# Kernel optimization log

Measured on AMD Instinct MI355X. Metric: run time of the kernel, lower is better.

## Reference

```python
import jax, jax.numpy as jnp
import numpy as np


def conv1x1(x, w, b):
    # x: (b,c,h,w), w: (o,c), b: (o,)
    return jnp.einsum('oc,bchw->bohw', w, x) + b[None, :, None, None]


def make_grid(b, h, w, outH, outW, scale, offset):
    # Replicates the torch grid construction (align_corners=True style normalization).
    gx = ((jnp.arange(outW, dtype=jnp.float32) + 0.5) / scale - 0.5) * 2.0 / (w - 1) - 1.0
    gy = ((jnp.arange(outH, dtype=jnp.float32) + 0.5) / scale - 0.5) * 2.0 / (h - 1) - 1.0
    ix = jnp.broadcast_to(gx[None, None, :], (b, outH, outW))
    iy = jnp.broadcast_to(gy[None, :, None], (b, outH, outW))
    if offset is not None:
        ix = ix + offset[:, 0] * 2.0 / (w - 1)
        iy = iy + offset[:, 1] * 2.0 / (h - 1)
    return ix, iy


def grid_sample_zeros(img, ix, iy):
    # Bilinear grid_sample, padding_mode='zeros', align_corners=False (torch default).
    b, c, h, w = img.shape
    fx = ((ix + 1.0) * w - 1.0) / 2.0
    fy = ((iy + 1.0) * h - 1.0) / 2.0
    x0 = jnp.floor(fx); y0 = jnp.floor(fy)
    x1 = x0 + 1.0; y1 = y0 + 1.0
    wx1 = fx - x0; wx0 = 1.0 - wx1
    wy1 = fy - y0; wy0 = 1.0 - wy1
    bidx = jnp.arange(b)[:, None, None]

    def gather(xc, yc):
        valid = (xc >= 0) & (xc <= w - 1) & (yc >= 0) & (yc <= h - 1)
        xi = jnp.clip(xc, 0, w - 1).astype(jnp.int32)
        yi = jnp.clip(yc, 0, h - 1).astype(jnp.int32)
        v = img[bidx, :, yi, xi]  # (b,H,W,c)
        return jnp.where(valid[..., None], v, 0.0)

    out = (gather(x0, y0) * (wx0 * wy0)[..., None]
           + gather(x1, y0) * (wx1 * wy0)[..., None]
           + gather(x0, y1) * (wx0 * wy1)[..., None]
           + gather(x1, y1) * (wx1 * wy1)[..., None])
    return jnp.transpose(out, (0, 3, 1, 2))  # (b,c,H,W)


def setup_inputs() -> dict:
    key = jax.random.key(0)
    C, E = 64, 4
    ks = jax.random.split(key, 12)
    s = 0.05
    return {
        'x': jax.random.normal(ks[0], (2, C, 128, 128), dtype=jnp.float32),
        'weight_compress': jax.random.normal(ks[1], (E, C // 8, C), dtype=jnp.float32) * s,
        'weight_expand': jax.random.normal(ks[2], (E, C, C // 8), dtype=jnp.float32) * s,
        'w1': jax.random.normal(ks[3], (C, C + 4), dtype=jnp.float32) * s,
        'b1': jax.random.normal(ks[4], (C,), dtype=jnp.float32) * s,
        'w2': jax.random.normal(ks[5], (C, C), dtype=jnp.float32) * s,
        'b2': jax.random.normal(ks[6], (C,), dtype=jnp.float32) * s,
        'wr': jax.random.normal(ks[7], (E, C), dtype=jnp.float32) * s,
        'br': jax.random.normal(ks[8], (E,), dtype=jnp.float32) * s,
        'wo': jax.random.normal(ks[9], (2, C), dtype=jnp.float32) * s,
        'bo': jax.random.normal(ks[10], (2,), dtype=jnp.float32) * s,
        'scale': 2,
        'outH': 256,
        'outW': 256,
    }


def reference(x, weight_compress, weight_expand, w1, b1, w2, b2, wr, br, wo, bo, scale, outH, outW):
    b, c, h, w = x.shape
    # relative sub-pixel coordinates
    ah = jnp.arange(outH, dtype=jnp.float32)
    aw = jnp.arange(outW, dtype=jnp.float32)
    coor_h = (ah + 0.5) / scale - jnp.floor((ah + 0.5) / scale + 0.001) - 0.5  # (outH,)
    coor_w = (aw + 0.5) / scale - jnp.floor((aw + 0.5) / scale + 0.001) - 0.5  # (outW,)
    ones_hw = jnp.full((outH, outW), 1.0 / scale, dtype=jnp.float32)
    coords = jnp.stack([ones_hw, ones_hw,
                        jnp.broadcast_to(coor_h[:, None], (outH, outW)),
                        jnp.broadcast_to(coor_w[None, :], (outH, outW))], axis=0)  # (4,H,W)
    coords = jnp.broadcast_to(coords[None], (b, 4, outH, outW))

    ix, iy = make_grid(b, h, w, outH, outW, scale, None)
    pre_fea = grid_sample_zeros(x, ix, iy)  # (b,C,H,W)

    inp = jnp.concatenate([coords, pre_fea], axis=1)  # (b,C+4,H,W)
    emb = jax.nn.relu(conv1x1(jax.nn.relu(conv1x1(inp, w1, b1)), w2, b2))

    offset = conv1x1(emb, wo, bo)  # (b,2,H,W)
    ix2, iy2 = make_grid(b, h, w, outH, outW, scale, offset)
    fea0 = grid_sample_zeros(x, ix2, iy2)  # (b,C,H,W)

    r = jax.nn.sigmoid(conv1x1(emb, wr, br))  # (b,E,H,W) routing weights
    # per-pixel expert-blended compress->expand (algebraically identical to
    # materializing per-pixel weight matrices, but as E small GEMM pairs)
    comp = jnp.einsum('behw,edc,bchw->bdhw', r, weight_compress, fea0)  # (b,C/8,H,W)
    out = jnp.einsum('behw,ecd,bdhw->bchw', r, weight_expand, comp)    # (b,C,H,W)
    return out + fea0
```

## Files before the change

### kernel.cpp

```cpp
#include <hip/hip_runtime.h>
#include <math.h>

#define BATCH 2
#define C 64
#define HIN 128
#define WIN 128
#define HW (HIN * WIN)
#define OH 256
#define OW 256

#define BLK 256
#define PIX 64
#define SC 16
#define ASTR 72
#define YSTR 36
#define OSTR 68


typedef __attribute__((ext_vector_type(8))) short bf16x8;
typedef __attribute__((ext_vector_type(4))) float f32x4;

__device__ __forceinline__ unsigned short f2bf(float f) {
    unsigned u = __float_as_uint(f);
    u += 0x7FFFu + ((u >> 16) & 1u);
    return (unsigned short)(u >> 16);
}
__device__ __forceinline__ float bf2f(unsigned short s) {
    return __uint_as_float(((unsigned)s) << 16);
}

__device__ __forceinline__ void bilin_setup(float gx, float gy,
    int& i00, int& i10, int& i01, int& i11,
    float& w00, float& w10, float& w01, float& w11)
{
    const float fx = ((gx + 1.0f) * WIN - 1.0f) * 0.5f;
    const float fy = ((gy + 1.0f) * HIN - 1.0f) * 0.5f;
    const float x0 = floorf(fx), y0 = floorf(fy);
    const float wx1 = fx - x0, wx0 = 1.0f - wx1;
    const float wy1 = fy - y0, wy0 = 1.0f - wy1;
    const float x1 = x0 + 1.0f, y1 = y0 + 1.0f;
    const bool vx0 = (x0 >= 0.0f) && (x0 <= (float)(WIN - 1));
    const bool vx1 = (x1 >= 0.0f) && (x1 <= (float)(WIN - 1));
    const bool vy0 = (y0 >= 0.0f) && (y0 <= (float)(HIN - 1));
    const bool vy1 = (y1 >= 0.0f) && (y1 <= (float)(HIN - 1));
    const int xi0 = (int)fminf(fmaxf(x0, 0.0f), (float)(WIN - 1));
    const int xi1 = (int)fminf(fmaxf(x1, 0.0f), (float)(WIN - 1));
    const int yi0 = (int)fminf(fmaxf(y0, 0.0f), (float)(HIN - 1));
    const int yi1 = (int)fminf(fmaxf(y1, 0.0f), (float)(HIN - 1));
    w00 = wx0 * wy0 * ((vx0 && vy0) ? 1.0f : 0.0f);
    w10 = wx1 * wy0 * ((vx1 && vy0) ? 1.0f : 0.0f);
    w01 = wx0 * wy1 * ((vx0 && vy1) ? 1.0f : 0.0f);
    w11 = wx1 * wy1 * ((vx1 && vy1) ? 1.0f : 0.0f);
    i00 = yi0 * WIN + xi0;  i10 = yi0 * WIN + xi1;
    i01 = yi1 * WIN + xi0;  i11 = yi1 * WIN + xi1;
}

__global__ __launch_bounds__(BLK, 4) void scab_kernel(
    const float* __restrict__ x,
    const float* __restrict__ wcm,
    const float* __restrict__ wex,
    const float* __restrict__ w1,
    const float* __restrict__ b1,
    const float* __restrict__ w2,
    const float* __restrict__ b2,
    const float* __restrict__ wr,
    const float* __restrict__ br,
    const float* __restrict__ wo,
    const float* __restrict__ bo,
    float* __restrict__ out)
{
    __shared__ __align__(16) short act[PIX * ASTR];
    __shared__ __align__(16) float red[PIX * OSTR];

    const int tid  = threadIdx.x;
    const int lane = tid & 63;
    const int s    = __builtin_amdgcn_readfirstlane(tid >> 6);
    const int cb   = s * SC;
    const int l15  = lane & 15;
    const int quad = lane >> 4;
    const int nn   = cb + l15;

    const int gp = blockIdx.x * PIX + lane;
    const int ox = gp & (OW - 1);
    const int oy = (gp >> 8) & (OH - 1);
    const int bb = gp >> 16;

    const float gx = ((ox + 0.5f) * 0.5f - 0.5f) * (2.0f / (WIN - 1)) - 1.0f;
    const float gy = ((oy + 0.5f) * 0.5f - 0.5f) * (2.0f / (HIN - 1)) - 1.0f;

    const float* __restrict__ xb = x + bb * (C * HW);

    bf16x8 bw1[2], bw2[2], bwc[2], bwe;
    {
        const int nt1  = s & 1;
        const int eo_g = nt1 * 16 + l15;
        #pragma unroll
        for (int ks = 0; ks < 2; ++ks) {
            const float* __restrict__ s1p = w1 + nn * (C + 4) + 4 + ks * 32 + quad * 8;
            const float* __restrict__ s2p = w2 + nn * C + ks * 32 + quad * 8;
            const float* __restrict__ scp = wcm + eo_g * C + ks * 32 + quad * 8;
            #pragma unroll
            for (int j = 0; j < 8; ++j) {
                bw1[ks][j] = (short)f2bf(s1p[j]);
                bw2[ks][j] = (short)f2bf(s2p[j]);
                bwc[ks][j] = (short)f2bf(scp[j]);
            }
        }
        const float* __restrict__ sep = wex + (quad * C + nn) * 8;
        #pragma unroll
        for (int j = 0; j < 8; ++j) bwe[j] = (short)f2bf(sep[j]);
    }

    {
        int i00, i10, i01, i11;
        float w00, w10, w01, w11;
        bilin_setup(gx, gy, i00, i10, i01, i11, w00, w10, w01, w11);
        bf16x8 v0, v1;
        #pragma unroll
        for (int kk = 0; kk < SC; kk += 4) {
            float l[16];
            #pragma unroll
            for (int k = 0; k < 4; ++k) {
                const float* __restrict__ xc = xb + (cb + kk + k) * HW;
                l[4*k+0] = xc[i00]; l[4*k+1] = xc[i10];
                l[4*k+2] = xc[i01]; l[4*k+3] = xc[i11];
            }
            #pragma unroll
            for (int k = 0; k < 4; ++k) {
                const float pf = l[4*k]*w00 + l[4*k+1]*w10 + l[4*k+2]*w01 + l[4*k+3]*w11;
                const short b = (short)f2bf(pf);
                if (kk + k < 8) v0[kk + k] = b; else v1[kk + k - 8] = b;
            }
        }
        *(bf16x8*)&act[lane * ASTR + cb]     = v0;
        *(bf16x8*)&act[lane * ASTR + cb + 8] = v1;
    }
    __syncthreads();

    const float coor_h = (oy & 1) ? 0.25f : -0.25f;
    f32x4 acc[4];
    {
        const float4 wh = *(const float4*)(w1 + nn * (C + 4));
        const float qn = b1[nn] + (wh.x + wh.y) * 0.5f + wh.z * coor_h;
        const float e0 = qn - 0.25f * wh.w;
        const float e1 = qn + 0.25f * wh.w;
        #pragma unroll
        for (int t = 0; t < 4; ++t) acc[t] = (f32x4){e0, e1, e0, e1};
    }
    #pragma unroll
    for (int t = 0; t < 4; ++t) {
        #pragma unroll
        for (int ks = 0; ks < 2; ++ks) {
            const bf16x8 af = *(const bf16x8*)&act[(t*16 + l15) * ASTR + ks*32 + quad*8];
            acc[t] = __builtin_amdgcn_mfma_f32_16x16x32_bf16(af, bw1[ks], acc[t], 0, 0, 0);
        }
    }
    __syncthreads();
    #pragma unroll
    for (int t = 0; t < 4; ++t)
        #pragma unroll
        for (int r = 0; r < 4; ++r)
            act[(t*16 + quad*4 + r) * ASTR + nn] = (short)f2bf(fmaxf(acc[t][r], 0.0f));
    __syncthreads();

    {
        const float b2n = b2[nn];
        #pragma unroll
        for (int t = 0; t < 4; ++t) acc[t] = (f32x4){b2n, b2n, b2n, b2n};
    }
    #pragma unroll
    for (int t = 0; t < 4; ++t) {
        #pragma unroll
        for (int ks = 0; ks < 2; ++ks) {
            const bf16x8 af = *(const bf16x8*)&act[(t*16 + l15) * ASTR + ks*32 + quad*8];
            acc[t] = __builtin_amdgcn_mfma_f32_16x16x32_bf16(af, bw2[ks], acc[t], 0, 0, 0);
        }
    }
    __syncthreads();
    #pragma unroll
    for (int t = 0; t < 4; ++t)
        #pragma unroll
        for (int r = 0; r < 4; ++r)
            act[(t*16 + quad*4 + r) * ASTR + nn] = (short)f2bf(fmaxf(acc[t][r], 0.0f));
    __syncthreads();

    float hx = 0.0f, hy = 0.0f, z0p = 0.0f, z1p = 0.0f, z2p = 0.0f, z3p = 0.0f;
    {
        const bf16x8 u0 = *(const bf16x8*)&act[lane * ASTR + cb];
        const bf16x8 u1 = *(const bf16x8*)&act[lane * ASTR + cb + 8];
        #pragma unroll
        for (int k = 0; k < SC; ++k) {
            const int o = cb + k;
            const float e = bf2f((unsigned short)(k < 8 ? u0[k] : u1[k - 8]));
            hx  = fmaf(wo[o],         e, hx);
            hy  = fmaf(wo[C + o],     e, hy);
            z0p = fmaf(wr[o],         e, z0p);
            z1p = fmaf(wr[C + o],     e, z1p);
            z2p = fmaf(wr[2 * C + o], e, z2p);
            z3p = fmaf(wr[3 * C + o], e, z3p);
        }
    }
    red[0 * 256 + s * 64 + lane] = hx;
    red[1 * 256 + s * 64 + lane] = hy;
    red[2 * 256 + s * 64 + lane] = z0p;
    red[3 * 256 + s * 64 + lane] = z1p;
    red[4 * 256 + s * 64 + lane] = z2p;
    red[5 * 256 + s * 64 + lane] = z3p;
    __syncthreads();

    float offx = bo[0], offy = bo[1];
    float z0 = br[0], z1 = br[1], z2 = br[2], z3 = br[3];
    #pragma unroll
    for (int ss = 0; ss < 4; ++ss) {
        offx += red[0 * 256 + ss * 64 + lane];
        offy += red[1 * 256 + ss * 64 + lane];
        z0   += red[2 * 256 + ss * 64 + lane];
        z1   += red[3 * 256 + ss * 64 + lane];
        z2   += red[4 * 256 + ss * 64 + lane];
        z3   += red[5 * 256 + ss * 64 + lane];
    }
    const float rg0 = 1.0f / (1.0f + __expf(-z0));
    const float rg1 = 1.0f / (1.0f + __expf(-z1));
    const float rg2 = 1.0f / (1.0f + __expf(-z2));
    const float rg3 = 1.0f / (1.0f + __expf(-z3));

    float f[SC];
    {
        int j00, j10, j01, j11;
        float v00, v10, v01, v11;
        bilin_setup(gx + offx * (2.0f / (WIN - 1)),
                    gy + offy * (2.0f / (HIN - 1)),
                    j00, j10, j01, j11, v00, v10, v01, v11);
        bf16x8 v0, v1;
        #pragma unroll
        for (int kk = 0; kk < SC; kk += 4) {
            float l[16];
            #pragma unroll
            for (int k = 0; k < 4; ++k) {
                const float* __restrict__ xc = xb + (cb + kk + k) * HW;
                l[4*k+0] = xc[j00]; l[4*k+1] = xc[j10];
                l[4*k+2] = xc[j01]; l[4*k+3] = xc[j11];
            }
            #pragma unroll
            for (int k = 0; k < 4; ++k) {
                const float fc = l[4*k]*v00 + l[4*k+1]*v10 + l[4*k+2]*v01 + l[4*k+3]*v11;
                f[kk + k] = fc;
                const short b = (short)f2bf(fc);
                if (kk + k < 8) v0[kk + k] = b; else v1[kk + k - 8] = b;
            }
        }
        *(bf16x8*)&act[lane * ASTR + cb]     = v0;
        *(bf16x8*)&act[lane * ASTR + cb + 8] = v1;
    }
    __syncthreads();

    {
        const int nt1 = s & 1;
        const int mb  = (s >> 1) * 2;
        #pragma unroll
        for (int mi = 0; mi < 2; ++mi) {
            const int mt = mb + mi;
            f32x4 yac = (f32x4){0.0f, 0.0f, 0.0f, 0.0f};
            #pragma unroll
            for (int ks = 0; ks < 2; ++ks) {
                const bf16x8 af = *(const bf16x8*)&act[(mt*16 + l15) * ASTR + ks*32 + quad*8];
                yac = __builtin_amdgcn_mfma_f32_16x16x32_bf16(af, bwc[ks], yac, 0, 0, 0);
            }
            #pragma unroll
            for (int r = 0; r < 4; ++r)
                red[(mt*16 + quad*4 + r) * YSTR + nt1*16 + l15] = yac[r];
        }
    }
    __syncthreads();

    {
        float comp[8];
        const float* __restrict__ yr = &red[lane * YSTR];
        #pragma unroll
        for (int d = 0; d < 8; ++d) {
            float v = rg0 * yr[d];
            v = fmaf(rg1, yr[8 + d],  v);
            v = fmaf(rg2, yr[16 + d], v);
            v = fmaf(rg3, yr[24 + d], v);
            comp[d] = v;
        }
        bf16x8 t0, t1, t2, t3;
        #pragma unroll
        for (int d = 0; d < 8; ++d) {
            t0[d] = (short)f2bf(rg0 * comp[d]);
            t1[d] = (short)f2bf(rg1 * comp[d]);
            t2[d] = (short)f2bf(rg2 * comp[d]);
            t3[d] = (short)f2bf(rg3 * comp[d]);
        }
        __syncthreads();
        *(bf16x8*)&act[lane * ASTR + 0]  = t0;
        *(bf16x8*)&act[lane * ASTR + 8]  = t1;
        *(bf16x8*)&act[lane * ASTR + 16] = t2;
        *(bf16x8*)&act[lane * ASTR + 24] = t3;
    }
    __syncthreads();

    #pragma unroll
    for (int t = 0; t < 4; ++t) {
        f32x4 oac = (f32x4){0.0f, 0.0f, 0.0f, 0.0f};
        const bf16x8 af = *(const bf16x8*)&act[(t*16 + l15) * ASTR + quad*8];
        oac = __builtin_amdgcn_mfma_f32_16x16x32_bf16(af, bwe, oac, 0, 0, 0);
        #pragma unroll
        for (int r = 0; r < 4; ++r)
            red[(t*16 + quad*4 + r) * OSTR + nn] = oac[r];
    }
    __syncthreads();

    float* __restrict__ ob = out + bb * (C * OH * OW) + oy * OW + ox;
    const float* __restrict__ orow = &red[lane * OSTR + cb];
    #pragma unroll
    for (int kk = 0; kk < SC; kk += 4) {
        const float4 e4 = *(const float4*)(orow + kk);
        ob[(cb + kk + 0) * (OH * OW)] = f[kk + 0] + e4.x;
        ob[(cb + kk + 1) * (OH * OW)] = f[kk + 1] + e4.y;
        ob[(cb + kk + 2) * (OH * OW)] = f[kk + 2] + e4.z;
        ob[(cb + kk + 3) * (OH * OW)] = f[kk + 3] + e4.w;
    }
}

extern "C" void kernel_launch(void* const* d_in, const int* in_sizes, int n_in,
                              void* d_out, int out_size, void* d_ws, size_t ws_size,
                              hipStream_t stream) {
    const float* x   = (const float*)d_in[0];
    const float* wcm = (const float*)d_in[1];
    const float* wex = (const float*)d_in[2];
    const float* w1  = (const float*)d_in[3];
    const float* b1  = (const float*)d_in[4];
    const float* w2  = (const float*)d_in[5];
    const float* b2  = (const float*)d_in[6];
    const float* wr  = (const float*)d_in[7];
    const float* br  = (const float*)d_in[8];
    const float* wo  = (const float*)d_in[9];
    const float* bo  = (const float*)d_in[10];
    float* out = (float*)d_out;

    const int total  = BATCH * OH * OW;
    const int blocks = total / PIX;
    scab_kernel<<<blocks, BLK, 0, stream>>>(x, wcm, wex, w1, b1, w2, b2,
                                            wr, br, wo, bo, out);
}
```

Baseline: 119.3 us.

## Pre-convert weights to bf16 in workspace and compute offset/routing heads with MFMA

Adds a prep kernel that converts all weight matrices to bf16 once per call into the workspace, so each block loads packed bf16x8 vectors instead of converting fp32 scalars. The per-wave scalar offset and routing dot products, along with their cross-wave shared-memory reduction, are replaced by one padded 16-column MFMA head per wave. A redundant barrier in the expand stage is also removed. In exchange there is an extra kernel launch and bf16 precision for the offset and routing head weights.

```diff
diff --git a/kernel.cpp b/kernel.cpp
--- a/kernel.cpp
+++ b/kernel.cpp
@@ -13,8 +13,15 @@
 #define PIX 64
 #define SC 16
 #define ASTR 72
-#define YSTR 36
+#define YHSTR 17
+#define YSTR 33
 #define OSTR 68
+
+#define WS_W2  4096
+#define WS_WC  8192
+#define WS_WE  10240
+#define WS_WH  12288
+#define WS_TOT 13312
 
 
 typedef __attribute__((ext_vector_type(8))) short bf16x8;
@@ -24,9 +31,6 @@
     unsigned u = __float_as_uint(f);
     u += 0x7FFFu + ((u >> 16) & 1u);
     return (unsigned short)(u >> 16);
-}
-__device__ __forceinline__ float bf2f(unsigned short s) {
-    return __uint_as_float(((unsigned)s) << 16);
 }
 
 __device__ __forceinline__ void bilin_setup(float gx, float gy,
@@ -55,18 +59,40 @@
     i01 = yi1 * WIN + xi0;  i11 = yi1 * WIN + xi1;
 }
 
+__global__ __launch_bounds__(256) void prep_kernel(
+    const float* __restrict__ wcm, const float* __restrict__ wex,
+    const float* __restrict__ w1,  const float* __restrict__ w2,
+    const float* __restrict__ wr,  const float* __restrict__ wo,
+    unsigned short* __restrict__ wsb)
+{
+    const int i = blockIdx.x * 256 + threadIdx.x;
+    if (i >= WS_TOT) return;
+    float v = 0.0f;
+    if (i < WS_W2) {
+        const int n = i >> 6, k = i & 63;
+        v = w1[n * (C + 4) + 4 + k];
+    } else if (i < WS_WC) {
+        v = w2[i - WS_W2];
+    } else if (i < WS_WE) {
+        v = wcm[i - WS_WC];
+    } else if (i < WS_WH) {
+        v = wex[i - WS_WE];
+    } else {
+        const int j = i - WS_WH;
+        const int n = j >> 6, k = j & 63;
+        v = (n < 2) ? wo[n * C + k] : ((n < 6) ? wr[(n - 2) * C + k] : 0.0f);
+    }
+    wsb[i] = f2bf(v);
+}
+
 __global__ __launch_bounds__(BLK, 4) void scab_kernel(
     const float* __restrict__ x,
-    const float* __restrict__ wcm,
-    const float* __restrict__ wex,
     const float* __restrict__ w1,
     const float* __restrict__ b1,
-    const float* __restrict__ w2,
     const float* __restrict__ b2,
-    const float* __restrict__ wr,
     const float* __restrict__ br,
-    const float* __restrict__ wo,
     const float* __restrict__ bo,
+    const unsigned short* __restrict__ wsb,
     float* __restrict__ out)
 {
     __shared__ __align__(16) short act[PIX * ASTR];
@@ -90,26 +116,17 @@
 
     const float* __restrict__ xb = x + bb * (C * HW);
 
-    bf16x8 bw1[2], bw2[2], bwc[2], bwe;
-    {
-        const int nt1  = s & 1;
-        const int eo_g = nt1 * 16 + l15;
-        #pragma unroll
-        for (int ks = 0; ks < 2; ++ks) {
-            const float* __restrict__ s1p = w1 + nn * (C + 4) + 4 + ks * 32 + quad * 8;
-            const float* __restrict__ s2p = w2 + nn * C + ks * 32 + quad * 8;
-            const float* __restrict__ scp = wcm + eo_g * C + ks * 32 + quad * 8;
-            #pragma unroll
-            for (int j = 0; j < 8; ++j) {
-                bw1[ks][j] = (short)f2bf(s1p[j]);
-                bw2[ks][j] = (short)f2bf(s2p[j]);
-                bwc[ks][j] = (short)f2bf(scp[j]);
-            }
-        }
-        const float* __restrict__ sep = wex + (quad * C + nn) * 8;
-        #pragma unroll
-        for (int j = 0; j < 8; ++j) bwe[j] = (short)f2bf(sep[j]);
-    }
+    const int nt1  = s & 1;
+    const int eo_g = nt1 * 16 + l15;
+    bf16x8 bw1[2], bw2[2], bwc[2], bhd[2], bwe;
+    #pragma unroll
+    for (int ks = 0; ks < 2; ++ks) {
+        bw1[ks] = *(const bf16x8*)(wsb +         nn   * 64 + ks * 32 + quad * 8);
+        bw2[ks] = *(const bf16x8*)(wsb + WS_W2 + nn   * 64 + ks * 32 + quad * 8);
+        bwc[ks] = *(const bf16x8*)(wsb + WS_WC + eo_g * 64 + ks * 32 + quad * 8);
+        bhd[ks] = *(const bf16x8*)(wsb + WS_WH + l15  * 64 + ks * 32 + quad * 8);
+    }
+    bwe = *(const bf16x8*)(wsb + WS_WE + (quad * C + nn) * 8);
 
     {
         int i00, i10, i01, i11;
@@ -184,45 +201,26 @@
             act[(t*16 + quad*4 + r) * ASTR + nn] = (short)f2bf(fmaxf(acc[t][r], 0.0f));
     __syncthreads();
 
-    float hx = 0.0f, hy = 0.0f, z0p = 0.0f, z1p = 0.0f, z2p = 0.0f, z3p = 0.0f;
-    {
-        const bf16x8 u0 = *(const bf16x8*)&act[lane * ASTR + cb];
-        const bf16x8 u1 = *(const bf16x8*)&act[lane * ASTR + cb + 8];
-        #pragma unroll
-        for (int k = 0; k < SC; ++k) {
-            const int o = cb + k;
-            const float e = bf2f((unsigned short)(k < 8 ? u0[k] : u1[k - 8]));
-            hx  = fmaf(wo[o],         e, hx);
-            hy  = fmaf(wo[C + o],     e, hy);
-            z0p = fmaf(wr[o],         e, z0p);
-            z1p = fmaf(wr[C + o],     e, z1p);
-            z2p = fmaf(wr[2 * C + o], e, z2p);
-            z3p = fmaf(wr[3 * C + o], e, z3p);
-        }
-    }
-    red[0 * 256 + s * 64 + lane] = hx;
-    red[1 * 256 + s * 64 + lane] = hy;
-    red[2 * 256 + s * 64 + lane] = z0p;
-    red[3 * 256 + s * 64 + lane] = z1p;
-    red[4 * 256 + s * 64 + lane] = z2p;
-    red[5 * 256 + s * 64 + lane] = z3p;
-    __syncthreads();
-
-    float offx = bo[0], offy = bo[1];
-    float z0 = br[0], z1 = br[1], z2 = br[2], z3 = br[3];
-    #pragma unroll
-    for (int ss = 0; ss < 4; ++ss) {
-        offx += red[0 * 256 + ss * 64 + lane];
-        offy += red[1 * 256 + ss * 64 + lane];
-        z0   += red[2 * 256 + ss * 64 + lane];
-        z1   += red[3 * 256 + ss * 64 + lane];
-        z2   += red[4 * 256 + ss * 64 + lane];
-        z3   += red[5 * 256 + ss * 64 + lane];
-    }
-    const float rg0 = 1.0f / (1.0f + __expf(-z0));
-    const float rg1 = 1.0f / (1.0f + __expf(-z1));
-    const float rg2 = 1.0f / (1.0f + __expf(-z2));
-    const float rg3 = 1.0f / (1.0f + __expf(-z3));
+    {
+        f32x4 yac = (f32x4){0.0f, 0.0f, 0.0f, 0.0f};
+        #pragma unroll
+        for (int ks = 0; ks < 2; ++ks) {
+            const bf16x8 af = *(const bf16x8*)&act[(s*16 + l15) * ASTR + ks*32 + quad*8];
+            yac = __builtin_amdgcn_mfma_f32_16x16x32_bf16(af, bhd[ks], yac, 0, 0, 0);
+        }
+        #pragma unroll
+        for (int r = 0; r < 4; ++r)
+            red[(s*16 + quad*4 + r) * YHSTR + l15] = yac[r];
+    }
+    __syncthreads();
+
+    const float* __restrict__ yp = &red[lane * YHSTR];
+    const float offx = bo[0] + yp[0];
+    const float offy = bo[1] + yp[1];
+    const float rg0 = 1.0f / (1.0f + __expf(-(br[0] + yp[2])));
+    const float rg1 = 1.0f / (1.0f + __expf(-(br[1] + yp[3])));
+    const float rg2 = 1.0f / (1.0f + __expf(-(br[2] + yp[4])));
+    const float rg3 = 1.0f / (1.0f + __expf(-(br[3] + yp[5])));
 
     float f[SC];
     {
@@ -255,8 +253,7 @@
     __syncthreads();
 
     {
-        const int nt1 = s & 1;
-        const int mb  = (s >> 1) * 2;
+        const int mb = (s >> 1) * 2;
         #pragma unroll
         for (int mi = 0; mi < 2; ++mi) {
             const int mt = mb + mi;
@@ -284,15 +281,18 @@
             v = fmaf(rg3, yr[24 + d], v);
             comp[d] = v;
         }
-        bf16x8 t0, t1, t2, t3;
+        bf16x8 t0, t1;
         #pragma unroll
         for (int d = 0; d < 8; ++d) {
             t0[d] = (short)f2bf(rg0 * comp[d]);
             t1[d] = (short)f2bf(rg1 * comp[d]);
+        }
+        bf16x8 t2, t3;
+        #pragma unroll
+        for (int d = 0; d < 8; ++d) {
             t2[d] = (short)f2bf(rg2 * comp[d]);
             t3[d] = (short)f2bf(rg3 * comp[d]);
         }
-        __syncthreads();
         *(bf16x8*)&act[lane * ASTR + 0]  = t0;
         *(bf16x8*)&act[lane * ASTR + 8]  = t1;
         *(bf16x8*)&act[lane * ASTR + 16] = t2;
@@ -338,9 +338,11 @@
     const float* wo  = (const float*)d_in[9];
     const float* bo  = (const float*)d_in[10];
     float* out = (float*)d_out;
+    unsigned short* wsb = (unsigned short*)d_ws;
+
+    prep_kernel<<<(WS_TOT + 255) / 256, 256, 0, stream>>>(wcm, wex, w1, w2, wr, wo, wsb);
 
     const int total  = BATCH * OH * OW;
     const int blocks = total / PIX;
-    scab_kernel<<<blocks, BLK, 0, stream>>>(x, wcm, wex, w1, b1, w2, b2,
-                                            wr, br, wo, bo, out);
-}
+    scab_kernel<<<blocks, BLK, 0, stream>>>(x, w1, b1, b2, br, bo, wsb, out);
+}
```

Measured after the change: 118.0 us. No clear change (-1.1%).
